# Performance work log

Measured on AMD Instinct MI355X. Metric: run time of the kernel, lower is better.

Reference implementation:

```python
import jax, jax.numpy as jnp
import numpy as np

D_MODEL = 1024
NUM_HEADS = 8
HEAD_DIM = D_MODEL // NUM_HEADS


def setup_inputs() -> dict:
    key = jax.random.key(0)
    ks = jax.random.split(key, 9)
    B, Ld, Le = 4, 1024, 2048
    s = 1.0 / np.sqrt(D_MODEL)
    return {
        "mhca_input": jax.random.normal(ks[0], (B, Ld, D_MODEL), jnp.float32),
        "encoder_output": jax.random.normal(ks[1], (B, Le, D_MODEL), jnp.float32),
        "cross_mask": jnp.zeros((B, Ld, Le), jnp.float32),
        "W_kv": jax.random.normal(ks[2], (2 * D_MODEL, D_MODEL), jnp.float32) * s,
        "b_kv": jnp.zeros((2 * D_MODEL,), jnp.float32),
        "W_q": jax.random.normal(ks[3], (D_MODEL, D_MODEL), jnp.float32) * s,
        "b_q": jnp.zeros((D_MODEL,), jnp.float32),
        "W_o": jax.random.normal(ks[4], (D_MODEL, D_MODEL), jnp.float32) * s,
        "b_o": jnp.zeros((D_MODEL,), jnp.float32),
    }


def _mhca(x, enc, mask, W_kv, b_kv, W_q, b_q, W_o, b_o):
    B, Ld, _ = x.shape
    Le = enc.shape[1]
    kv = enc @ W_kv.T + b_kv                      # [B, Le, 2*d_model]
    q = x @ W_q.T + b_q                           # [B, Ld, d_model]
    kv = kv.reshape(B, Le, NUM_HEADS, 2 * HEAD_DIM).transpose(0, 2, 1, 3)
    q = q.reshape(B, Ld, NUM_HEADS, HEAD_DIM).transpose(0, 2, 1, 3)
    k, v = kv[..., :HEAD_DIM], kv[..., HEAD_DIM:]
    scaled = jnp.einsum("bhqd,bhkd->bhqk", q, k) / np.sqrt(HEAD_DIM)
    if mask is not None:
        scaled = scaled + mask[:, None, :, :]     # == permute/add/permute in torch
    attn = jax.nn.softmax(scaled, axis=-1)
    vals = jnp.einsum("bhqk,bhkd->bhqd", attn, v)
    vals = vals.transpose(0, 2, 1, 3).reshape(B, Ld, D_MODEL)
    return vals @ W_o.T + b_o


def reference(mhca_input, encoder_output, cross_mask, W_kv, b_kv, W_q, b_q, W_o, b_o):
    return _mhca(mhca_input, encoder_output, cross_mask, W_kv, b_kv, W_q, b_q, W_o, b_o)
```

## Files before the change

kernel.cpp:

```cpp
#include <hip/hip_runtime.h>
#include <hip/hip_bf16.h>
#include <stdint.h>


#define DM   1024
#define NH   8
#define HD   128
#define LDQ  1024
#define LE   2048
#define NB   4

typedef __attribute__((ext_vector_type(8))) short bf16x8;
typedef __attribute__((ext_vector_type(4))) float f32x4;

__device__ __forceinline__ unsigned short f2bf(float f) {
  union { float f; uint32_t u; } v; v.f = f;
  uint32_t u = v.u + 0x7fffu + ((v.u >> 16) & 1u);
  return (unsigned short)(u >> 16);
}
__device__ __forceinline__ float bf2f(unsigned short u) {
  union { uint32_t u; float f; } v; v.u = ((uint32_t)u) << 16;
  return v.f;
}

__device__ __forceinline__ void gl_lds16(const void* g, void* l) {
  __builtin_amdgcn_global_load_lds(
      (const __attribute__((address_space(1))) void*)g,
      (__attribute__((address_space(3))) void*)l, 16, 0, 0);
}

__global__ void init_flag_kernel(int* flag) { if (threadIdx.x == 0) *flag = 0; }

__global__ __launch_bounds__(256) void scan_mask_kernel(const float* __restrict__ m,
                                                        int* __restrict__ flag, int n4) {
  int i = blockIdx.x * blockDim.x + threadIdx.x;
  int stride = gridDim.x * blockDim.x;
  int nz = 0;
  for (; i < n4; i += stride) {
    float4 v = ((const float4*)m)[i];
    nz |= (v.x != 0.f) | (v.y != 0.f) | (v.z != 0.f) | (v.w != 0.f);
  }
  if (nz) atomicOr(flag, 1);
}

__global__ __launch_bounds__(256) void cvt_all_kernel(
    const float* __restrict__ s0, const float* __restrict__ s1,
    const float* __restrict__ s2, const float* __restrict__ s3,
    const float* __restrict__ s4, const float* __restrict__ s5,
    unsigned short* __restrict__ d0, unsigned short* __restrict__ d1,
    unsigned short* __restrict__ d2, unsigned short* __restrict__ d3,
    unsigned short* __restrict__ d4, unsigned short* __restrict__ d5,
    int* __restrict__ flag, int do_mask) {
  const int total = 6291456;
  int i = blockIdx.x * blockDim.x + threadIdx.x;
  int stride = gridDim.x * blockDim.x;
  for (; i < total; i += stride) {
    const float* src; unsigned short* dst; int off; float sub = 0.f; int ismask = 0;
    if (i < 1048576)      { src = s0; dst = d0; off = i; }
    else if (i < 3145728) { src = s1; dst = d1; off = i - 1048576; }
    else if (i < 3407872) { src = s2; dst = d2; off = i - 3145728; }
    else if (i < 3932160) { src = s3; dst = d3; off = i - 3407872; }
    else if (i < 4194304) { src = s4; dst = d4; off = i - 3932160; }
    else { if (!do_mask) continue; src = s5; dst = d5; off = i - 4194304; sub = 8.0f; ismask = 1; }
    float4 v = ((const float4*)src)[off];
    if (ismask && ((v.x != 0.f) | (v.y != 0.f) | (v.z != 0.f) | (v.w != 0.f)))
      atomicOr(flag, 1);
    ushort4 o;
    o.x = f2bf(v.x - sub); o.y = f2bf(v.y - sub);
    o.z = f2bf(v.z - sub); o.w = f2bf(v.w - sub);
    ((ushort4*)dst)[off] = o;
  }
}

template <int MODE>
__global__ __launch_bounds__(256) void gemm_bt(const unsigned short* __restrict__ A,
                                               const unsigned short* __restrict__ B,
                                               const float* __restrict__ bias,
                                               unsigned short* __restrict__ out0,
                                               unsigned short* __restrict__ out1,
                                               float* __restrict__ outf,
                                               int M, int N, int K) {
  __shared__ __align__(16) unsigned short As[2][128 * 32];
  __shared__ __align__(16) unsigned short Bs[2][128 * 32];
  const int tid = threadIdx.x;
  const int wave = tid >> 6, lane = tid & 63;
  const int wr = wave >> 1, wc = wave & 1;
  const int g = lane >> 4, c = lane & 15;
  const int m0 = blockIdx.y * 128, n0 = blockIdx.x * 128;

  f32x4 acc[4][4];
#pragma unroll
  for (int i = 0; i < 4; ++i)
#pragma unroll
    for (int j = 0; j < 4; ++j) acc[i][j] = (f32x4){0.f, 0.f, 0.f, 0.f};

  const unsigned short* Abase = A + (size_t)m0 * K;
  const unsigned short* Bbase = B + (size_t)n0 * K;

  auto stage = [&](int buf, int kt) {
    const unsigned short* at = Abase + kt * 32;
    const unsigned short* bt = Bbase + kt * 32;
#pragma unroll
    for (int j = 0; j < 2; ++j) {
      int chunk = wave * 2 + j;
      int o = chunk * 1024 + lane * 16;
      int os = o ^ (((o >> 6) & 3) << 4);
      int e = os >> 1;
      int row = e >> 5, col = e & 31;
      gl_lds16(at + row * K + col, (char*)(&As[buf][0]) + chunk * 1024);
      gl_lds16(bt + row * K + col, (char*)(&Bs[buf][0]) + chunk * 1024);
    }
  };

  auto compute = [&](int buf) {
    bf16x8 af[4], bfr[4];
#pragma unroll
    for (int mi = 0; mi < 4; ++mi) {
      int row = wr * 64 + mi * 16 + c;
      int byte = (row * 64 + g * 16) ^ ((row & 3) << 4);
      af[mi] = *(const bf16x8*)((const char*)&As[buf][0] + byte);
    }
#pragma unroll
    for (int ni = 0; ni < 4; ++ni) {
      int row = wc * 64 + ni * 16 + c;
      int byte = (row * 64 + g * 16) ^ ((row & 3) << 4);
      bfr[ni] = *(const bf16x8*)((const char*)&Bs[buf][0] + byte);
    }
#pragma unroll
    for (int mi = 0; mi < 4; ++mi)
#pragma unroll
      for (int ni = 0; ni < 4; ++ni)
        acc[mi][ni] = __builtin_amdgcn_mfma_f32_16x16x32_bf16(af[mi], bfr[ni],
                                                              acc[mi][ni], 0, 0, 0);
  };

  const int NT = K >> 5;
  stage(0, 0);
  __syncthreads();
  int cur = 0;
  for (int t = 0; t < NT; ++t) {
    if (t + 1 < NT) stage(cur ^ 1, t + 1);
    compute(cur);
    __syncthreads();
    cur ^= 1;
  }

#pragma unroll
  for (int mi = 0; mi < 4; ++mi) {
#pragma unroll
    for (int ni = 0; ni < 4; ++ni) {
      int n = n0 + wc * 64 + ni * 16 + c;
      float bv = bias[n];
#pragma unroll
      for (int r = 0; r < 4; ++r) {
        int m = m0 + wr * 64 + mi * 16 + g * 4 + r;
        float val = acc[mi][ni][r] + bv;
        if constexpr (MODE == 0) {
          val *= 0.08838834764831845f;
          int b = m >> 10, ld = m & 1023, h = n >> 7, d = n & 127;
          out0[((size_t)((b * 8 + h) * 1024 + ld)) * 128 + d] = f2bf(val);
        } else if constexpr (MODE == 1) {
          int b = m >> 11, le = m & 2047, h = n >> 8, w2 = n & 255;
          if (w2 < 128)
            out0[((size_t)((b * 8 + h) * 2048 + le)) * 128 + w2] = f2bf(val);
          else
            out1[((size_t)((b * 8 + h) * 128 + (w2 - 128))) * 2048 + le] = f2bf(val);
        } else {
          outf[(size_t)m * 1024 + n] = val;
        }
      }
    }
  }
}

template <int MBF>
__global__ __launch_bounds__(512, 2) void attn_kernel(const unsigned short* __restrict__ q,
                                                      const unsigned short* __restrict__ k,
                                                      const unsigned short* __restrict__ vT,
                                                      const void* __restrict__ maskp,
                                                      const int* __restrict__ flagp,
                                                      unsigned short* __restrict__ att) {
  __shared__ __align__(16) unsigned short Ks[2][2][64 * 128];
  __shared__ __align__(16) unsigned short Vs[2][2][128 * 64];
  __shared__ __align__(16) unsigned short Ps[8][16 * 64];

  const int tid = threadIdx.x, wave = tid >> 6, lane = tid & 63;
  const int wsub = wave & 3, kvh = wave >> 2;
  const int g = lane >> 4, c = lane & 15;
  const int bid = blockIdx.x;
  const int xslot = bid & 7, slot = bid >> 3;

  const unsigned short* mb16 = (const unsigned short*)maskp;
  const float* mb32 = (const float*)maskp;
  const int has_mask = *flagp;

  bf16x8 ones;
#pragma unroll
  for (int i = 0; i < 8; ++i) ones[i] = (c == 0) ? (short)0x3F80 : (short)0;

  for (int ph = 0; ph < 2; ++ph) {
    const int bh = xslot + 8 * (2 * ph + (slot >> 4));
    const int b = bh >> 3, h = bh & 7;
    const int q0 = (slot & 15) * 64;

    const unsigned short* qbase = q + (size_t)bh * LDQ * HD + (size_t)q0 * HD;
    const unsigned short* kbase = k + (size_t)bh * LE * HD;
    const unsigned short* vbase = vT + (size_t)bh * HD * LE;
    const size_t mrowbase = ((size_t)b * LDQ + q0);

    bf16x8 qf[4];
    {
      const int qrow = wsub * 16 + c;
#pragma unroll
      for (int kc = 0; kc < 4; ++kc)
        qf[kc] = *(const bf16x8*)(qbase + (size_t)qrow * HD + kc * 32 + g * 8);
    }

    auto stage_kv = [&](int buf, int tg) {
#pragma unroll
      for (int j = 0; j < 4; ++j) {
        int chunk = wsub * 4 + j;
        int o = chunk * 1024 + lane * 16;
        int osk = o ^ (((o >> 8) & 7) << 4);
        gl_lds16(kbase + (size_t)tg * 64 * HD + (osk >> 1),
                 (char*)&Ks[kvh][buf][0] + chunk * 1024);
        int osv = o ^ (((o >> 7) & 7) << 4);
        int e = osv >> 1;
        int d = e >> 6, kvo = e & 63;
        gl_lds16(vbase + (size_t)d * LE + tg * 64 + kvo,
                 (char*)&Vs[kvh][buf][0] + chunk * 1024);
      }
    };

    float mcur[16], mnext[16];
    auto load_mask = [&](int tg, float* mr) {
#pragma unroll
      for (int n = 0; n < 4; ++n)
#pragma unroll
        for (int r = 0; r < 4; ++r) {
          size_t idx = (mrowbase + wsub * 16 + g * 4 + r) * LE + tg * 64 + n * 16 + c;
          if constexpr (MBF) mr[n * 4 + r] = bf2f(mb16[idx]);
          else               mr[n * 4 + r] = mb32[idx] - 8.0f;
        }
    };

    f32x4 o_acc[8];
    f32x4 o_l = (f32x4){0.f, 0.f, 0.f, 0.f};
#pragma unroll
    for (int i = 0; i < 8; ++i) o_acc[i] = (f32x4){0.f, 0.f, 0.f, 0.f};

    __syncthreads();
    stage_kv(0, kvh);
    if (has_mask) load_mask(kvh, mcur);
    else {
#pragma unroll
      for (int i = 0; i < 16; ++i) mcur[i] = -8.0f;
    }
    __syncthreads();

    const int NT2 = LE / 128;
    int buf = 0;
    for (int t = 0; t < NT2; ++t) {
      if (t + 1 < NT2) {
        stage_kv(buf ^ 1, 2 * (t + 1) + kvh);
        if (has_mask) load_mask(2 * (t + 1) + kvh, mnext);
      }

      f32x4 s[4];
#pragma unroll
      for (int n = 0; n < 4; ++n) s[n] = (f32x4){0.f, 0.f, 0.f, 0.f};
#pragma unroll
      for (int kc = 0; kc < 4; ++kc) {
#pragma unroll
        for (int n = 0; n < 4; ++n) {
          int kv = n * 16 + c;
          int byte = (kv * 256 + kc * 64 + g * 16) ^ ((kv & 7) << 4);
          bf16x8 kf = *(const bf16x8*)((const char*)&Ks[kvh][buf][0] + byte);
          s[n] = __builtin_amdgcn_mfma_f32_16x16x32_bf16(qf[kc], kf, s[n], 0, 0, 0);
        }
      }

#pragma unroll
      for (int n = 0; n < 4; ++n)
#pragma unroll
        for (int r = 0; r < 4; ++r) {
          float p = __expf(s[n][r] + mcur[n * 4 + r]);
          int row = g * 4 + r;
          int byte = (row * 128 + (n * 16 + c) * 2) ^ ((row & 7) << 4);
          *(unsigned short*)((char*)&Ps[wave][0] + byte) = f2bf(p);
        }
      asm volatile("s_waitcnt lgkmcnt(0)" ::: "memory");
      __builtin_amdgcn_sched_barrier(0);

#pragma unroll
      for (int kc2 = 0; kc2 < 2; ++kc2) {
        int pb = (c * 128 + kc2 * 64 + g * 16) ^ ((c & 7) << 4);
        bf16x8 pa = *(const bf16x8*)((const char*)&Ps[wave][0] + pb);
        o_l = __builtin_amdgcn_mfma_f32_16x16x32_bf16(pa, ones, o_l, 0, 0, 0);
#pragma unroll
        for (int dn = 0; dn < 8; ++dn) {
          int d = dn * 16 + c;
          int byte = (d * 128 + kc2 * 64 + g * 16) ^ ((d & 7) << 4);
          bf16x8 vf = *(const bf16x8*)((const char*)&Vs[kvh][buf][0] + byte);
          o_acc[dn] = __builtin_amdgcn_mfma_f32_16x16x32_bf16(pa, vf, o_acc[dn], 0, 0, 0);
        }
      }

      __syncthreads();
      buf ^= 1;
      if (has_mask) {
#pragma unroll
        for (int i = 0; i < 16; ++i) mcur[i] = mnext[i];
      }
    }

    float l[4];
#pragma unroll
    for (int r = 0; r < 4; ++r) l[r] = __shfl(o_l[r], lane & 48);

    float* osc = (float*)&Ks[0][0][0];
    float* lsc = (float*)&Vs[0][0][0];
    if (kvh == 1) {
#pragma unroll
      for (int dn = 0; dn < 8; ++dn)
#pragma unroll
        for (int r = 0; r < 4; ++r)
          osc[(wsub * 16 + g * 4 + r) * 128 + dn * 16 + c] = o_acc[dn][r];
      if (c == 0) {
#pragma unroll
        for (int r = 0; r < 4; ++r) lsc[wsub * 16 + g * 4 + r] = l[r];
      }
    }
    __syncthreads();
    if (kvh == 0) {
#pragma unroll
      for (int r = 0; r < 4; ++r) {
        l[r] += lsc[wsub * 16 + g * 4 + r];
        l[r] = 1.0f / l[r];
      }
#pragma unroll
      for (int dn = 0; dn < 8; ++dn)
#pragma unroll
        for (int r = 0; r < 4; ++r) {
          float o = o_acc[dn][r] + osc[(wsub * 16 + g * 4 + r) * 128 + dn * 16 + c];
          int qrow = q0 + wsub * 16 + g * 4 + r;
          att[((size_t)(b * LDQ) + qrow) * DM + h * HD + dn * 16 + c] =
              f2bf(o * l[r]);
        }
    }
  }
}

extern "C" void kernel_launch(void* const* d_in, const int* in_sizes, int n_in,
                              void* d_out, int out_size, void* d_ws, size_t ws_size,
                              hipStream_t stream) {
  const float* x    = (const float*)d_in[0];
  const float* enc  = (const float*)d_in[1];
  const float* mask = (const float*)d_in[2];
  const float* Wkv  = (const float*)d_in[3];
  const float* bkv  = (const float*)d_in[4];
  const float* Wq   = (const float*)d_in[5];
  const float* bq   = (const float*)d_in[6];
  const float* Wo   = (const float*)d_in[7];
  const float* bo   = (const float*)d_in[8];
  float* out = (float*)d_out;

  char* ws = (char*)d_ws;
  int* flag = (int*)ws; ws += 16;
  unsigned short* x_bf    = (unsigned short*)ws; ws += (size_t)4096 * 1024 * 2;
  unsigned short* enc_bf  = (unsigned short*)ws; ws += (size_t)8192 * 1024 * 2;
  unsigned short* wq_bf   = (unsigned short*)ws; ws += (size_t)1024 * 1024 * 2;
  unsigned short* wkv_bf  = (unsigned short*)ws; ws += (size_t)2048 * 1024 * 2;
  unsigned short* wo_bf   = (unsigned short*)ws; ws += (size_t)1024 * 1024 * 2;
  unsigned short* q_bf    = (unsigned short*)ws; ws += (size_t)4096 * 1024 * 2;
  unsigned short* k_bf    = (unsigned short*)ws; ws += (size_t)8192 * 1024 * 2;
  unsigned short* vT_bf   = (unsigned short*)ws; ws += (size_t)8192 * 1024 * 2;
  unsigned short* att_bf  = (unsigned short*)ws; ws += (size_t)4096 * 1024 * 2;
  unsigned short* mask_bf = (unsigned short*)ws; ws += (size_t)8192 * 1024 * 2;

  const size_t need = (size_t)(ws - (char*)d_ws);
  const int use_bf_mask = (ws_size >= need) ? 1 : 0;

  init_flag_kernel<<<1, 64, 0, stream>>>(flag);
  if (!use_bf_mask)
    scan_mask_kernel<<<512, 256, 0, stream>>>(mask, flag, 2097152);

  cvt_all_kernel<<<2048, 256, 0, stream>>>(x, enc, Wq, Wkv, Wo, mask,
                                           x_bf, enc_bf, wq_bf, wkv_bf, wo_bf,
                                           mask_bf, flag, use_bf_mask);

  gemm_bt<0><<<dim3(8, 32), 256, 0, stream>>>(x_bf, wq_bf, bq, q_bf, nullptr, nullptr,
                                              4096, 1024, 1024);
  gemm_bt<1><<<dim3(16, 64), 256, 0, stream>>>(enc_bf, wkv_bf, bkv, k_bf, vT_bf, nullptr,
                                               8192, 2048, 1024);
  if (use_bf_mask)
    attn_kernel<1><<<256, 512, 0, stream>>>(q_bf, k_bf, vT_bf, mask_bf, flag, att_bf);
  else
    attn_kernel<0><<<256, 512, 0, stream>>>(q_bf, k_bf, vT_bf, mask, flag, att_bf);
  gemm_bt<2><<<dim3(8, 32), 256, 0, stream>>>(att_bf, wo_bf, bo, nullptr, nullptr, out,
                                              4096, 1024, 1024);
}
```

Before: 377.0 us.

## Prefetch two GEMM tiles ahead, remap workgroups, and stage V-transpose stores through LDS

The GEMM main loop now keeps two k-tiles in flight using explicit vmcnt waits and raw barriers, so global loads overlap more compute. Workgroup indices are remapped in groups of eight, likely to spread neighbouring tiles across XCDs and improve cache locality. For the KV projection, the transposed V output is first written into shared memory and then stored as coalesced 16-byte rows, replacing scattered 2-byte strided stores. The hand-written waitcnt values depend on the exact number of loads per stage and could break if the staging code changes.

```diff
diff --git a/kernel.cpp b/kernel.cpp
--- a/kernel.cpp
+++ b/kernel.cpp
@@ -86,7 +86,12 @@
   const int wave = tid >> 6, lane = tid & 63;
   const int wr = wave >> 1, wc = wave & 1;
   const int g = lane >> 4, c = lane & 15;
-  const int m0 = blockIdx.y * 128, n0 = blockIdx.x * 128;
+
+  const int gx = gridDim.x, nwg = gx * gridDim.y;
+  const int w0 = blockIdx.y * gx + blockIdx.x;
+  const int cpx = nwg >> 3;
+  const int sw = (w0 & 7) * cpx + (w0 >> 3);
+  const int m0 = (sw / gx) * 128, n0 = (sw % gx) * 128;
 
   f32x4 acc[4][4];
 #pragma unroll
@@ -136,15 +141,59 @@
 
   const int NT = K >> 5;
   stage(0, 0);
-  __syncthreads();
+  stage(1, 1);
+  asm volatile("s_waitcnt vmcnt(4)" ::: "memory");
+  __builtin_amdgcn_sched_barrier(0);
+  __builtin_amdgcn_s_barrier();
+
   int cur = 0;
   for (int t = 0; t < NT; ++t) {
-    if (t + 1 < NT) stage(cur ^ 1, t + 1);
     compute(cur);
-    __syncthreads();
+    asm volatile("s_waitcnt lgkmcnt(0)" ::: "memory");
+    __builtin_amdgcn_sched_barrier(0);
+    __builtin_amdgcn_s_barrier();
+    if (t + 2 < NT) {
+      stage(cur, t + 2);
+      asm volatile("s_waitcnt vmcnt(4)" ::: "memory");
+    } else {
+      asm volatile("s_waitcnt vmcnt(0)" ::: "memory");
+    }
+    __builtin_amdgcn_sched_barrier(0);
+    __builtin_amdgcn_s_barrier();
     cur ^= 1;
   }
 
+  if constexpr (MODE == 1) {
+    if (n0 & 128) {
+      char* half = (wc == 0) ? (char*)&As[0][0] : (char*)&Bs[0][0];
+#pragma unroll
+      for (int ni = 0; ni < 4; ++ni) {
+        int dl = ni * 16 + c;
+        int dsw = ((wc * 64 + ni * 16 + c) & 7) << 4;
+#pragma unroll
+        for (int mi = 0; mi < 4; ++mi)
+#pragma unroll
+          for (int r = 0; r < 4; ++r) {
+            int le = wr * 64 + mi * 16 + g * 4 + r;
+            float val = acc[mi][ni][r] + bias[n0 + wc * 64 + ni * 16 + c];
+            *(unsigned short*)(half + ((dl * 256 + le * 2) ^ dsw)) = f2bf(val);
+          }
+      }
+      __builtin_amdgcn_s_barrier();
+      const int b = m0 >> 11, h = (n0 >> 8) & 7;
+      unsigned short* vdst = out1 + ((size_t)(b * 8 + h) * 128) * 2048 + (m0 & 2047);
+#pragma unroll
+      for (int i = 0; i < 8; ++i) {
+        int o = i * 4096 + tid * 16;
+        int d = o >> 8, le8 = (o & 255) >> 1;
+        char* src = (d < 64) ? (char*)&As[0][0] : (char*)&Bs[0][0];
+        int byte = (((d & 63) * 256 + le8 * 2) ^ ((d & 7) << 4));
+        bf16x8 v = *(const bf16x8*)(src + byte);
+        *(bf16x8*)(vdst + (size_t)d * 2048 + le8) = v;
+      }
+      return;
+    }
+  }
 #pragma unroll
   for (int mi = 0; mi < 4; ++mi) {
 #pragma unroll
@@ -160,11 +209,8 @@
           int b = m >> 10, ld = m & 1023, h = n >> 7, d = n & 127;
           out0[((size_t)((b * 8 + h) * 1024 + ld)) * 128 + d] = f2bf(val);
         } else if constexpr (MODE == 1) {
-          int b = m >> 11, le = m & 2047, h = n >> 8, w2 = n & 255;
-          if (w2 < 128)
-            out0[((size_t)((b * 8 + h) * 2048 + le)) * 128 + w2] = f2bf(val);
-          else
-            out1[((size_t)((b * 8 + h) * 128 + (w2 - 128))) * 2048 + le] = f2bf(val);
+          int b = m >> 11, le = m & 2047, h = n >> 8, d = n & 127;
+          out0[((size_t)((b * 8 + h) * 2048 + le)) * 128 + d] = f2bf(val);
         } else {
           outf[(size_t)m * 1024 + n] = val;
         }
```

Measured after the change: 354.8 us. -5.9%, faster.
